# Kernel optimization log

Measured on AMD Instinct MI355X. Metric: run time of the kernel, lower is better.

## Reference

```python
import jax, jax.numpy as jnp
import numpy as np

B, S, H = 2, 2048, 1024
NH, HD = 16, 64  # num heads, head dim


def setup_inputs() -> dict:
    key = jax.random.key(0)
    ks = jax.random.split(key, 8)
    scale = 0.02
    return {
        "hidden_states": jax.random.normal(ks[0], (B, S, H), dtype=jnp.float32),
        "attention_mask": jnp.zeros((B, 1, 1, S), dtype=jnp.float32),
        "Wq": jax.random.normal(ks[1], (H, H), dtype=jnp.float32) * scale,
        "bq": jnp.zeros((H,), dtype=jnp.float32),
        "Wk": jax.random.normal(ks[2], (H, H), dtype=jnp.float32) * scale,
        "bk": jnp.zeros((H,), dtype=jnp.float32),
        "Wv": jax.random.normal(ks[3], (H, H), dtype=jnp.float32) * scale,
        "bv": jnp.zeros((H,), dtype=jnp.float32),
    }


def _split_heads(x):
    # [B,S,H] -> [B,NH,S,HD]
    b, s, _ = x.shape
    return x.reshape(b, s, NH, HD).transpose(0, 2, 1, 3)


def reference(hidden_states, attention_mask, Wq, bq, Wk, bk, Wv, bv):
    q = _split_heads(hidden_states @ Wq.T + bq)
    k = _split_heads(hidden_states @ Wk.T + bk)
    v = _split_heads(hidden_states @ Wv.T + bv)
    # scores: [B,NH,S,S]
    scores = jnp.einsum("bhqd,bhkd->bhqk", q, k) / jnp.sqrt(jnp.float32(HD))
    scores = scores + attention_mask
    att = jax.nn.softmax(scores, axis=-1)  # dropout is identity in eval
    ctx = jnp.einsum("bhqk,bhkd->bhqd", att, v)
    # [B,NH,S,HD] -> [B,S,H]
    return ctx.transpose(0, 2, 1, 3).reshape(hidden_states.shape[0], hidden_states.shape[1], NH * HD)
```

## Files before the change

kernel.cpp:

```cpp
#include <hip/hip_runtime.h>
#include <stdint.h>

#define BB 2
#define SS 2048
#define HH 1024
#define NH 16
#define HD 64

#define LOG2E 1.4426950408889634f
#define QSCALE (0.125f * LOG2E)

typedef short bfrag  __attribute__((ext_vector_type(8)));
typedef short bfrag4 __attribute__((ext_vector_type(4)));
typedef float f32x4  __attribute__((ext_vector_type(4)));

__device__ __forceinline__ short f2bf(float f) {
    union { float f; uint32_t u; } v; v.f = f;
    uint32_t r = (v.u + 0x7fffu + ((v.u >> 16) & 1u)) >> 16;
    return (short)r;
}

__global__ __launch_bounds__(256) void cvt_all(
    const float* __restrict__ X,  const float* __restrict__ Wq,
    const float* __restrict__ Wk, const float* __restrict__ Wv,
    const float* __restrict__ mask,
    short* __restrict__ Xb, short* __restrict__ Wcat,
    float* __restrict__ maskl)
{
    int i = blockIdx.x * 256 + threadIdx.x;
    if (i >= 1835008) {
        int off = i - 1835008;
        float4 f = ((const float4*)mask)[off];
        f.x *= LOG2E; f.y *= LOG2E; f.z *= LOG2E; f.w *= LOG2E;
        ((float4*)maskl)[off] = f;
        return;
    }
    const float* src; short* dst; int off;
    if (i < 1048576)      { src = X;  dst = Xb;                 off = i; }
    else if (i < 1310720) { src = Wq; dst = Wcat;               off = i - 1048576; }
    else if (i < 1572864) { src = Wk; dst = Wcat + 1048576;     off = i - 1310720; }
    else                  { src = Wv; dst = Wcat + 2097152;     off = i - 1572864; }
    float4 f = ((const float4*)src)[off];
    short4 s;
    s.x = f2bf(f.x); s.y = f2bf(f.y); s.z = f2bf(f.z); s.w = f2bf(f.w);
    ((short4*)dst)[off] = s;
}

__device__ __forceinline__ void gload_lds16(const void* g, void* lds) {
    __builtin_amdgcn_global_load_lds(
        (__attribute__((address_space(1))) void*)(uintptr_t)g,
        (__attribute__((address_space(3))) void*)(uintptr_t)lds,
        16, 0, 0);
}

__global__ __launch_bounds__(256, 3) void qkv_gemm(
    const short* __restrict__ X, const short* __restrict__ Wcat,
    const float* __restrict__ bq, const float* __restrict__ bk, const float* __restrict__ bv,
    short* __restrict__ Qo, short* __restrict__ Ko, short* __restrict__ Vo)
{
    __shared__ __align__(16) short smem[17408];

    const int tid  = threadIdx.x;
    const int wave = tid >> 6, lane = tid & 63;
    const int quad = lane >> 4, l15 = lane & 15;
    const int mTile = blockIdx.y * 128;
    const int nTile = blockIdx.x * 128;
    const int z = nTile >> 10;
    const int nLocT = nTile & 1023;
    const float* bias = (z == 0) ? bq : (z == 1) ? bk : bv;

    f32x4 acc[4][4];
#pragma unroll
    for (int i = 0; i < 4; ++i)
#pragma unroll
        for (int j = 0; j < 4; ++j) acc[i][j] = (f32x4)0.0f;

    const int srow  = lane >> 3;
    const int c_lin = lane & 7;
    const int mBase = (wave >> 1) * 64;
    const int nBase = (wave & 1) * 64;

    for (int k0 = 0; k0 < 1024; k0 += 64) {
        __syncthreads();
#pragma unroll
        for (int i = 0; i < 4; ++i) {
            int row = i * 32 + wave * 8 + srow;
            int cg  = c_lin ^ (row & 7);
            gload_lds16(X + (size_t)(mTile + row) * 1024 + k0 + cg * 8,
                        (char*)smem + i * 4096 + wave * 1024);
            gload_lds16(Wcat + (size_t)(nTile + row) * 1024 + k0 + cg * 8,
                        (char*)smem + 16384 + i * 4096 + wave * 1024);
        }
        __syncthreads();

#pragma unroll
        for (int kt = 0; kt < 2; ++kt) {
            bfrag af[4], bf[4];
#pragma unroll
            for (int t = 0; t < 4; ++t) {
                int arow = mBase + t * 16 + l15;
                int aslot = (kt * 4 + quad) ^ (arow & 7);
                af[t] = *(const bfrag*)((const char*)smem + arow * 128 + aslot * 16);
                int brow = nBase + t * 16 + l15;
                int bslot = (kt * 4 + quad) ^ (brow & 7);
                bf[t] = *(const bfrag*)((const char*)smem + 16384 + brow * 128 + bslot * 16);
            }
#pragma unroll
            for (int mt = 0; mt < 4; ++mt)
#pragma unroll
                for (int ct = 0; ct < 4; ++ct)
                    acc[mt][ct] = __builtin_amdgcn_mfma_f32_16x16x32_bf16(
                        af[mt], bf[ct], acc[mt][ct], 0, 0, 0);
        }
    }

    __syncthreads();
    const int b = mTile >> 11, sBase = mTile & 2047;

    if (z == 2) {
#pragma unroll
        for (int mt = 0; mt < 4; ++mt)
#pragma unroll
            for (int ct = 0; ct < 4; ++ct)
#pragma unroll
                for (int r = 0; r < 4; ++r) {
                    int nl = nBase + ct * 16 + l15;
                    int sl = mBase + mt * 16 + quad * 4 + r;
                    smem[nl * 136 + sl] = f2bf(acc[mt][ct][r] + bias[nLocT + nl]);
                }
        __syncthreads();
#pragma unroll
        for (int p = 0; p < 8; ++p) {
            int nl = p * 16 + (tid >> 4);
            int c  = tid & 15;
            bfrag v8 = *(const bfrag*)(smem + nl * 136 + c * 8);
            int ng = nLocT + nl, hh = ng >> 6, d = ng & 63;
            *(bfrag*)(Vo + ((size_t)(b * 16 + hh) * 64 + d) * 2048 + sBase + c * 8) = v8;
        }
    } else {
        short* Out = (z == 0) ? Qo : Ko;
        float scale = (z == 0) ? QSCALE : 1.0f;
#pragma unroll
        for (int mt = 0; mt < 4; ++mt)
#pragma unroll
            for (int ct = 0; ct < 4; ++ct)
#pragma unroll
                for (int r = 0; r < 4; ++r) {
                    int ml = mBase + mt * 16 + quad * 4 + r;
                    int nl = nBase + ct * 16 + l15;
                    smem[ml * 136 + nl] = f2bf((acc[mt][ct][r] + bias[nLocT + nl]) * scale);
                }
        __syncthreads();
#pragma unroll
        for (int p = 0; p < 8; ++p) {
            int ml = p * 16 + (tid >> 4);
            int c  = tid & 15;
            bfrag v8 = *(const bfrag*)(smem + ml * 136 + c * 8);
            int s  = sBase + ml;
            int nl = nLocT + c * 8, hh = nl >> 6, d = nl & 63;
            *(bfrag*)(Out + (((size_t)(b * 16 + hh) << 11) + s) * 64 + d) = v8;
        }
    }
}

__global__ __launch_bounds__(256, 4) void attn_kernel(
    const short* __restrict__ Qb, const short* __restrict__ Kb, const short* __restrict__ Vb,
    const float* __restrict__ maskl, float* __restrict__ out)
{
    __shared__ __align__(16) char smem[32768];

    const int tid  = threadIdx.x;
    const int wave = tid >> 6, lane = tid & 63;
    const int quad = lane >> 4, l15 = lane & 15;
    const int bh = blockIdx.y, b = bh >> 4, h = bh & 15;
    const int qBase = blockIdx.x * 64 + wave * 16;

    int ksrc[2], vsrc[2];
#pragma unroll
    for (int i = 0; i < 2; ++i) {
        int ci = wave * 128 + i * 64 + lane;
        int r = ci >> 3, c = ci & 7;
        int cs = (c ^ (r & 7)) * 16;
        ksrc[i] = r * 128  + cs;
        vsrc[i] = r * 4096 + cs;
    }
    const char* kPtr = (const char*)(Kb + (size_t)bh * SS * HD);
    const char* vPtr = (const char*)(Vb + (size_t)bh * HD * SS);
    const char* mSrc = (const char*)(maskl + b * SS) + quad * 16;

    const short* Qp = Qb + ((size_t)bh * SS + qBase) * HD;
    bfrag qf[2];
#pragma unroll
    for (int kt = 0; kt < 2; ++kt)
        qf[kt] = *(const bfrag*)(Qp + (size_t)l15 * HD + kt * 32 + quad * 8);

    int kAddr[2];
#pragma unroll
    for (int kt = 0; kt < 2; ++kt)
        kAddr[kt] = l15 * 128 + (((kt * 4 + quad) ^ (l15 & 7)) * 16);
    int vAddr[4];
#pragma unroll
    for (int ct = 0; ct < 4; ++ct)
        vAddr[ct] = 8192 + l15 * 128 + (((ct * 2 + (quad >> 1)) ^ (l15 & 7)) * 16) + (quad & 1) * 8;

    const f32x4 z4 = (f32x4)0.0f;
    const bfrag4 ones = {0x3F80, 0x3F80, 0x3F80, 0x3F80};

    f32x4 oacc[4], ol = z4;
#pragma unroll
    for (int dt = 0; dt < 4; ++dt) oacc[dt] = z4;

#pragma unroll
    for (int i = 0; i < 2; ++i) {
        gload_lds16(kPtr + ksrc[i], smem + wave * 2048 + i * 1024);
        gload_lds16(vPtr + vsrc[i], smem + 8192 + wave * 2048 + i * 1024);
    }
    kPtr += 8192; vPtr += 128;

    for (int j = 0; j < 32; ++j) {
        const int cur = (j & 1) << 14;
        __syncthreads();
        if (j < 31) {
            const int nxt = 16384 - cur;
#pragma unroll
            for (int i = 0; i < 2; ++i) {
                gload_lds16(kPtr + ksrc[i], smem + nxt + wave * 2048 + i * 1024);
                gload_lds16(vPtr + vsrc[i], smem + nxt + 8192 + wave * 2048 + i * 1024);
            }
            kPtr += 8192; vPtr += 128;
        }
        const char* base = smem + cur;

        f32x4 mvl[4];
#pragma unroll
        for (int ct = 0; ct < 4; ++ct)
            mvl[ct] = *(const f32x4*)(mSrc + ct * 64);
        mSrc += 256;

        f32x4 s[4];
#pragma unroll
        for (int ct = 0; ct < 4; ++ct) {
            bfrag kf0 = *(const bfrag*)(base + kAddr[0] + ct * 2048);
            bfrag kf1 = *(const bfrag*)(base + kAddr[1] + ct * 2048);
            s[ct] = __builtin_amdgcn_mfma_f32_16x16x32_bf16(kf0, qf[0], z4,    0, 0, 0);
            s[ct] = __builtin_amdgcn_mfma_f32_16x16x32_bf16(kf1, qf[1], s[ct], 0, 0, 0);
        }

        bfrag4 pf[4];
#pragma unroll
        for (int ct = 0; ct < 4; ++ct) {
            uint32_t a0 = __float_as_uint(__builtin_amdgcn_exp2f(s[ct][0] + mvl[ct][0])) + 0x8000u;
            uint32_t a1 = __float_as_uint(__builtin_amdgcn_exp2f(s[ct][1] + mvl[ct][1])) + 0x8000u;
            uint32_t a2 = __float_as_uint(__builtin_amdgcn_exp2f(s[ct][2] + mvl[ct][2])) + 0x8000u;
            uint32_t a3 = __float_as_uint(__builtin_amdgcn_exp2f(s[ct][3] + mvl[ct][3])) + 0x8000u;
            union { uint32_t u[2]; bfrag4 v; } cvt;
            cvt.u[0] = __builtin_amdgcn_perm(a1, a0, 0x07060302u);
            cvt.u[1] = __builtin_amdgcn_perm(a3, a2, 0x07060302u);
            pf[ct] = cvt.v;
        }

#pragma unroll
        for (int dt = 0; dt < 4; ++dt) {
#pragma unroll
            for (int ct = 0; ct < 4; ++ct) {
                bfrag4 vf = *(const bfrag4*)(base + vAddr[ct] + dt * 2048);
                oacc[dt] = __builtin_amdgcn_mfma_f32_16x16x16bf16_1k(pf[ct], vf, oacc[dt], 0, 0, 0);
            }
        }
#pragma unroll
        for (int ct = 0; ct < 4; ++ct)
            ol = __builtin_amdgcn_mfma_f32_16x16x16bf16_1k(pf[ct], ones, ol, 0, 0, 0);
    }

#pragma unroll
    for (int r = 0; r < 4; ++r) {
        float linv = 1.0f / ol[r];
        int qrow = qBase + quad * 4 + r;
#pragma unroll
        for (int dt = 0; dt < 4; ++dt)
            out[((size_t)(b * SS + qrow)) * HH + h * 64 + dt * 16 + l15] =
                oacc[dt][r] * linv;
    }
}

extern "C" void kernel_launch(void* const* d_in, const int* in_sizes, int n_in,
                              void* d_out, int out_size, void* d_ws, size_t ws_size,
                              hipStream_t stream) {
    const float* hs   = (const float*)d_in[0];
    const float* mask = (const float*)d_in[1];
    const float* Wq   = (const float*)d_in[2];
    const float* bq   = (const float*)d_in[3];
    const float* Wk   = (const float*)d_in[4];
    const float* bk   = (const float*)d_in[5];
    const float* Wv   = (const float*)d_in[6];
    const float* bv   = (const float*)d_in[7];
    float* out = (float*)d_out;

    char* ws = (char*)d_ws;
    short* Xb    = (short*)(ws);
    short* Wcat  = (short*)(ws + (8ull  << 20));
    short* Qb    = (short*)(ws + (14ull << 20));
    short* Kb    = (short*)(ws + (22ull << 20));
    short* Vb    = (short*)(ws + (30ull << 20));
    float* maskl = (float*)(ws + (38ull << 20));

    cvt_all<<<7172, 256, 0, stream>>>(hs, Wq, Wk, Wv, mask, Xb, Wcat, maskl);

    qkv_gemm<<<dim3(24, 32), 256, 0, stream>>>(Xb, Wcat, bq, bk, bv, Qb, Kb, Vb);

    attn_kernel<<<dim3(SS / 64, BB * NH), 256, 0, stream>>>(Qb, Kb, Vb, maskl, out);
}
```

Before: 171.8 us.

## Double-buffer QKV GEMM with K=32 tiles and unroll attention loop by two

The QKV projection GEMM moves from a single-buffered K=64 tile with two barriers per step to a double-buffered K=32 tile. The next tile is prefetched into LDS while MFMAs run on the current one, with a 4-way XOR swizzle. The attention loop is manually unrolled by two so the buffer offsets become compile-time constants and the pointer increments go away. The aim is to hide global-to-LDS latency in the GEMM and cut address arithmetic. The cost is twice as many iterations with half the work each, so barrier overhead per unit of compute goes up.

```diff
diff --git a/kernel.cpp b/kernel.cpp
--- a/kernel.cpp
+++ b/kernel.cpp
@@ -75,43 +75,55 @@
 #pragma unroll
         for (int j = 0; j < 4; ++j) acc[i][j] = (f32x4)0.0f;
 
-    const int srow  = lane >> 3;
-    const int c_lin = lane & 7;
     const int mBase = (wave >> 1) * 64;
     const int nBase = (wave & 1) * 64;
 
-    for (int k0 = 0; k0 < 1024; k0 += 64) {
+    int asrc[2];
+#pragma unroll
+    for (int i = 0; i < 2; ++i) {
+        int ci = (i * 4 + wave) * 64 + lane;
+        int r = ci >> 2, c = ci & 3;
+        asrc[i] = r * 2048 + ((c ^ (r & 3)) * 16);
+    }
+    const int dmaDst0 = wave * 1024;
+    const char* aBase = (const char*)X + (size_t)mTile * 2048;
+    const char* bBase = (const char*)Wcat + (size_t)nTile * 2048;
+
+    const int aAddr = (mBase + l15) * 64 + ((quad ^ (l15 & 3)) * 16);
+    const int bAddr = (nBase + l15) * 64 + ((quad ^ (l15 & 3)) * 16);
+
+#pragma unroll
+    for (int i = 0; i < 2; ++i) {
+        gload_lds16(aBase + asrc[i], (char*)smem + dmaDst0 + i * 4096);
+        gload_lds16(bBase + asrc[i], (char*)smem + 8192 + dmaDst0 + i * 4096);
+    }
+
+    auto qstep = [&](int CUR, int NXT, int koffN, int pref) {
         __syncthreads();
-#pragma unroll
-        for (int i = 0; i < 4; ++i) {
-            int row = i * 32 + wave * 8 + srow;
-            int cg  = c_lin ^ (row & 7);
-            gload_lds16(X + (size_t)(mTile + row) * 1024 + k0 + cg * 8,
-                        (char*)smem + i * 4096 + wave * 1024);
-            gload_lds16(Wcat + (size_t)(nTile + row) * 1024 + k0 + cg * 8,
-                        (char*)smem + 16384 + i * 4096 + wave * 1024);
-        }
-        __syncthreads();
-
-#pragma unroll
-        for (int kt = 0; kt < 2; ++kt) {
-            bfrag af[4], bf[4];
-#pragma unroll
-            for (int t = 0; t < 4; ++t) {
-                int arow = mBase + t * 16 + l15;
-                int aslot = (kt * 4 + quad) ^ (arow & 7);
-                af[t] = *(const bfrag*)((const char*)smem + arow * 128 + aslot * 16);
-                int brow = nBase + t * 16 + l15;
-                int bslot = (kt * 4 + quad) ^ (brow & 7);
-                bf[t] = *(const bfrag*)((const char*)smem + 16384 + brow * 128 + bslot * 16);
+        if (pref) {
+#pragma unroll
+            for (int i = 0; i < 2; ++i) {
+                gload_lds16(aBase + koffN + asrc[i], (char*)smem + NXT + dmaDst0 + i * 4096);
+                gload_lds16(bBase + koffN + asrc[i], (char*)smem + NXT + 8192 + dmaDst0 + i * 4096);
             }
-#pragma unroll
-            for (int mt = 0; mt < 4; ++mt)
-#pragma unroll
-                for (int ct = 0; ct < 4; ++ct)
-                    acc[mt][ct] = __builtin_amdgcn_mfma_f32_16x16x32_bf16(
-                        af[mt], bf[ct], acc[mt][ct], 0, 0, 0);
-        }
+        }
+        bfrag af[4], bf[4];
+#pragma unroll
+        for (int t = 0; t < 4; ++t) {
+            af[t] = *(const bfrag*)((const char*)smem + CUR + aAddr + t * 1024);
+            bf[t] = *(const bfrag*)((const char*)smem + CUR + 8192 + bAddr + t * 1024);
+        }
+#pragma unroll
+        for (int mt = 0; mt < 4; ++mt)
+#pragma unroll
+            for (int ct = 0; ct < 4; ++ct)
+                acc[mt][ct] = __builtin_amdgcn_mfma_f32_16x16x32_bf16(
+                    af[mt], bf[ct], acc[mt][ct], 0, 0, 0);
+    };
+
+    for (int kk = 0; kk < 16; ++kk) {
+        qstep(0,     16384, (2 * kk + 1) * 64, 1);
+        qstep(16384, 0,     (2 * kk + 2) * 64, kk < 15);
     }
 
     __syncthreads();
@@ -184,9 +196,9 @@
         ksrc[i] = r * 128  + cs;
         vsrc[i] = r * 4096 + cs;
     }
-    const char* kPtr = (const char*)(Kb + (size_t)bh * SS * HD);
-    const char* vPtr = (const char*)(Vb + (size_t)bh * HD * SS);
-    const char* mSrc = (const char*)(maskl + b * SS) + quad * 16;
+    const char* kBase = (const char*)(Kb + (size_t)bh * SS * HD);
+    const char* vBase = (const char*)(Vb + (size_t)bh * HD * SS);
+    const char* mSrc  = (const char*)(maskl + b * SS) + quad * 16;
 
     const short* Qp = Qb + ((size_t)bh * SS + qBase) * HD;
     bfrag qf[2];
@@ -212,24 +224,19 @@
 
 #pragma unroll
     for (int i = 0; i < 2; ++i) {
-        gload_lds16(kPtr + ksrc[i], smem + wave * 2048 + i * 1024);
-        gload_lds16(vPtr + vsrc[i], smem + 8192 + wave * 2048 + i * 1024);
-    }
-    kPtr += 8192; vPtr += 128;
-
-    for (int j = 0; j < 32; ++j) {
-        const int cur = (j & 1) << 14;
+        gload_lds16(kBase + ksrc[i], smem + wave * 2048 + i * 1024);
+        gload_lds16(vBase + vsrc[i], smem + 8192 + wave * 2048 + i * 1024);
+    }
+
+    auto astep = [&](int CUR, int NXT, int jn, int pref) {
         __syncthreads();
-        if (j < 31) {
-            const int nxt = 16384 - cur;
+        if (pref) {
 #pragma unroll
             for (int i = 0; i < 2; ++i) {
-                gload_lds16(kPtr + ksrc[i], smem + nxt + wave * 2048 + i * 1024);
-                gload_lds16(vPtr + vsrc[i], smem + nxt + 8192 + wave * 2048 + i * 1024);
+                gload_lds16(kBase + jn * 8192 + ksrc[i], smem + NXT + wave * 2048 + i * 1024);
+                gload_lds16(vBase + jn * 128  + vsrc[i], smem + NXT + 8192 + wave * 2048 + i * 1024);
             }
-            kPtr += 8192; vPtr += 128;
-        }
-        const char* base = smem + cur;
+        }
 
         f32x4 mvl[4];
 #pragma unroll
@@ -240,8 +247,8 @@
         f32x4 s[4];
 #pragma unroll
         for (int ct = 0; ct < 4; ++ct) {
-            bfrag kf0 = *(const bfrag*)(base + kAddr[0] + ct * 2048);
-            bfrag kf1 = *(const bfrag*)(base + kAddr[1] + ct * 2048);
+            bfrag kf0 = *(const bfrag*)(smem + CUR + kAddr[0] + ct * 2048);
+            bfrag kf1 = *(const bfrag*)(smem + CUR + kAddr[1] + ct * 2048);
             s[ct] = __builtin_amdgcn_mfma_f32_16x16x32_bf16(kf0, qf[0], z4,    0, 0, 0);
             s[ct] = __builtin_amdgcn_mfma_f32_16x16x32_bf16(kf1, qf[1], s[ct], 0, 0, 0);
         }
@@ -263,13 +270,18 @@
         for (int dt = 0; dt < 4; ++dt) {
 #pragma unroll
             for (int ct = 0; ct < 4; ++ct) {
-                bfrag4 vf = *(const bfrag4*)(base + vAddr[ct] + dt * 2048);
+                bfrag4 vf = *(const bfrag4*)(smem + CUR + vAddr[ct] + dt * 2048);
                 oacc[dt] = __builtin_amdgcn_mfma_f32_16x16x16bf16_1k(pf[ct], vf, oacc[dt], 0, 0, 0);
             }
         }
 #pragma unroll
         for (int ct = 0; ct < 4; ++ct)
             ol = __builtin_amdgcn_mfma_f32_16x16x16bf16_1k(pf[ct], ones, ol, 0, 0, 0);
+    };
+
+    for (int jj = 0; jj < 16; ++jj) {
+        astep(0,     16384, 2 * jj + 1, 1);
+        astep(16384, 0,     2 * jj + 2, jj < 15);
     }
 
 #pragma unroll
```

Result: slower. 175.7 us (+2.2%).
